# Kernel tuning notes

Hardware: AMD Instinct MI355X
Metric: run time of the kernel (lower is better)

Reference implementation:

```python
import jax, jax.numpy as jnp
import numpy as np

L, D, H, KS, VS, HID = 2048, 1024, 16, 1024, 1024, 4096
EPS = 1e-5


def _linear_params(key, din, dout):
    # torch nn.Linear default init: U(-1/sqrt(din), 1/sqrt(din))
    s = 1.0 / np.sqrt(din)
    kw, kb = jax.random.split(key)
    W = jax.random.uniform(kw, (dout, din), minval=-s, maxval=s, dtype=jnp.float32)
    b = jax.random.uniform(kb, (dout,), minval=-s, maxval=s, dtype=jnp.float32)
    return W, b


def setup_inputs() -> dict:
    key = jax.random.key(0)
    ks = jax.random.split(key, 12)
    x = jax.random.normal(ks[0], (L, D), dtype=jnp.float32)
    # inverse shortest-path lengths in [0, 1]
    shortest_path = jax.random.uniform(ks[1], (L, L), dtype=jnp.float32)
    Wq, bq = _linear_params(ks[2], D, KS)
    Wk, bk = _linear_params(ks[3], D, KS)
    Wv, bv = _linear_params(ks[4], D, VS)
    Wqp, bqp = _linear_params(ks[5], KS, KS)
    Wkp, bkp = _linear_params(ks[6], KS, KS)
    Wvp, bvp = _linear_params(ks[7], VS, VS)
    Wo, bo = _linear_params(ks[8], VS, D)
    W1, b1 = _linear_params(ks[9], D, HID)
    W2, b2 = _linear_params(ks[10], HID, D)
    g1 = jnp.ones((D,), jnp.float32); be1 = jnp.zeros((D,), jnp.float32)
    g2 = jnp.ones((D,), jnp.float32); be2 = jnp.zeros((D,), jnp.float32)
    return dict(x=x, shortest_path=shortest_path,
                Wq=Wq, bq=bq, Wk=Wk, bk=bk, Wv=Wv, bv=bv,
                Wqp=Wqp, bqp=bqp, Wkp=Wkp, bkp=bkp, Wvp=Wvp, bvp=bvp,
                Wo=Wo, bo=bo, W1=W1, b1=b1, W2=W2, b2=b2,
                g1=g1, be1=be1, g2=g2, be2=be2)


def _dense(h, W, b):
    return h @ W.T + b


def _layernorm(h, g, b):
    mu = jnp.mean(h, axis=-1, keepdims=True)
    var = jnp.mean(jnp.square(h - mu), axis=-1, keepdims=True)
    return (h - mu) * jax.lax.rsqrt(var + EPS) * g + b


def reference(x, shortest_path, Wq, bq, Wk, bk, Wv, bv, Wqp, bqp, Wkp, bkp,
              Wvp, bvp, Wo, bo, W1, b1, W2, b2, g1, be1, g2, be2):
    hd = KS // H
    vhd = VS // H
    q = _dense(_dense(x, Wq, bq), Wqp, bqp).reshape(L, H, hd).transpose(1, 0, 2)   # [H,L,hd]
    k = _dense(_dense(x, Wk, bk), Wkp, bkp).reshape(L, H, hd).transpose(1, 0, 2)   # [H,L,hd]
    v = _dense(_dense(x, Wv, bv), Wvp, bvp).reshape(L, H, vhd).transpose(1, 0, 2)  # [H,L,vhd]
    att = jnp.einsum('hld,hmd->hlm', q, k) / jnp.sqrt(jnp.float32(hd))             # [H,L,L]
    sp_bias = jax.nn.softmax(shortest_path, axis=-1) * 0.5                          # [L,L]
    att = jax.nn.softmax(att + sp_bias[None, :, :], axis=-1)
    o = jnp.einsum('hlm,hmd->hld', att, v).transpose(1, 0, 2).reshape(L, VS)        # [L,VS]
    o = _dense(o, Wo, bo)
    h = _layernorm(x + o, g1, be1)                # residual + LN1 (dropout=identity)
    f = jax.nn.relu(_dense(jax.nn.relu(_dense(h, W1, b1)), W2, b2))
    return _layernorm(h + f, g2, be2)             # residual + LN2
```

## Files before the change

### kernel.cpp

```cpp
#include <hip/hip_runtime.h>

typedef __attribute__((ext_vector_type(4))) float f32x4;
typedef __attribute__((ext_vector_type(8))) short s16x8;

static __device__ __forceinline__ ushort f2b(float f) {
  union { float f; unsigned u; } v; v.f = f;
  unsigned u = v.u;
  unsigned r = (u + 0x7fffu + ((u >> 16) & 1u)) >> 16;
  return (ushort)r;
}
static __device__ __forceinline__ float b2f(ushort h) {
  union { unsigned u; float f; } v; v.u = ((unsigned)h) << 16;
  return v.f;
}
static __device__ __forceinline__ unsigned cvtpk(float a, float b) {
  unsigned r;
  asm("v_cvt_pk_bf16_f32 %0, %1, %2" : "=v"(r) : "v"(a), "v"(b));
  return r;
}
static __device__ __forceinline__ float exp2i(float x) {
  float r;
  asm("v_exp_f32 %0, %1" : "=v"(r) : "v"(x));
  return r;
}

static __device__ __forceinline__ void gload_lds16(const ushort* g, ushort* l) {
  __builtin_amdgcn_global_load_lds(
      (const __attribute__((address_space(1))) void*)g,
      (__attribute__((address_space(3))) void*)l, 16, 0, 0);
}

#define LOG2E 1.44269504f

struct Cvt7 {
  const float* src[7];
  ushort* dst[7];
  int n[7];
};
__global__ __launch_bounds__(256) void cvt_multi_k(Cvt7 a) {
  int e = blockIdx.y;
  int i = (blockIdx.x * 256 + threadIdx.x) * 4;
  if (i >= a.n[e]) return;
  float4 v4 = *(const float4*)(a.src[e] + i);
  ushort4 o4; o4.x = f2b(v4.x); o4.y = f2b(v4.y); o4.z = f2b(v4.z); o4.w = f2b(v4.w);
  *(ushort4*)(a.dst[e] + i) = o4;
}

__global__ __launch_bounds__(256) void wtr_k(const float* __restrict__ Wq,
                                             const float* __restrict__ Wk,
                                             const float* __restrict__ Wv,
                                             ushort* __restrict__ dst) {
  __shared__ float t[64][65];
  int z = blockIdx.z;
  const float* src = z == 0 ? Wq : (z == 1 ? Wk : Wv);
  float scale = z == 0 ? 0.125f * LOG2E : 1.f;
  int r0 = blockIdx.x * 64, c0 = blockIdx.y * 64;
  int lr = threadIdx.x >> 2, lc4 = (threadIdx.x & 3) * 16;
#pragma unroll
  for (int j = 0; j < 4; ++j)
    *(float4*)&t[lr][lc4 + j * 4] = *(const float4*)(src + (size_t)(r0 + lr) * 1024 + c0 + lc4 + j * 4);
  __syncthreads();
  ushort tmp[16];
#pragma unroll
  for (int j = 0; j < 16; ++j) tmp[j] = f2b(t[lc4 + j][lr] * scale);
  ushort* d = dst + (size_t)z * 1048576 + (size_t)(c0 + lr) * 1024 + r0 + lc4;
  *(uint4*)d = *(uint4*)tmp;
  *(uint4*)(d + 8) = *(uint4*)(tmp + 8);
}

__global__ __launch_bounds__(256) void bvec_k(
    const float* __restrict__ Wqp, const float* __restrict__ Wkp, const float* __restrict__ Wvp,
    const float* __restrict__ bq, const float* __restrict__ bqp,
    const float* __restrict__ bk, const float* __restrict__ bkp,
    const float* __restrict__ bv, const float* __restrict__ bvp,
    float* __restrict__ outb) {
  int r = blockIdx.x * 4 + (threadIdx.x >> 6);
  int lane = threadIdx.x & 63;
  int z = r >> 10, rr = r & 1023;
  const float* Wp = z == 0 ? Wqp : (z == 1 ? Wkp : Wvp);
  const float* bi = z == 0 ? bq : (z == 1 ? bk : bv);
  const float* bp = z == 0 ? bqp : (z == 1 ? bkp : bvp);
  float s = 0.f;
#pragma unroll
  for (int t = 0; t < 4; ++t) {
    float4 w = *(const float4*)(Wp + (size_t)rr * 1024 + lane * 16 + t * 4);
    float4 b = *(const float4*)(bi + lane * 16 + t * 4);
    s += w.x * b.x + w.y * b.y + w.z * b.z + w.w * b.w;
  }
#pragma unroll
  for (int m = 1; m < 64; m <<= 1) s += __shfl_xor(s, m);
  if (lane == 0) outb[r] = (s + bp[rr]) * (z == 0 ? 0.125f * LOG2E : 1.f);
}

__global__ __launch_bounds__(256) void spsm_k(const float* __restrict__ sp,
                                              ushort* __restrict__ outP) {
  const int Lc = 2048;
  int row = blockIdx.x;
  int tid = threadIdx.x;
  const float* r = sp + (size_t)row * Lc;
  float v[8];
  float mx = -1e30f;
#pragma unroll
  for (int j = 0; j < 8; ++j) { v[j] = r[tid + j * 256]; mx = fmaxf(mx, v[j]); }
#pragma unroll
  for (int m = 1; m < 64; m <<= 1) mx = fmaxf(mx, __shfl_xor(mx, m));
  __shared__ float redm[4], reds[4];
  if ((tid & 63) == 0) redm[tid >> 6] = mx;
  __syncthreads();
  mx = fmaxf(fmaxf(redm[0], redm[1]), fmaxf(redm[2], redm[3]));
  float s = 0.f;
#pragma unroll
  for (int j = 0; j < 8; ++j) { v[j] = __expf(v[j] - mx); s += v[j]; }
#pragma unroll
  for (int m = 1; m < 64; m <<= 1) s += __shfl_xor(s, m);
  if ((tid & 63) == 0) reds[tid >> 6] = s;
  __syncthreads();
  s = reds[0] + reds[1] + reds[2] + reds[3];
  float inv = 0.5f * LOG2E / s;
  int mb = row >> 6, rr = row & 63;
  int wv = rr >> 4, rem = rr & 15, rg = rem >> 2, ii = rem & 3;
  size_t rbase = ((size_t)mb * 32) * 4096 + (size_t)wv * 1024 + (size_t)ii * 256 + (size_t)rg * 16;
#pragma unroll
  for (int j = 0; j < 8; ++j) {
    int col = tid + j * 256;
    int nb = col >> 6, cc = col & 63, nt = cc >> 4, cl = cc & 15;
    outP[rbase + (size_t)nb * 4096 + nt * 64 + cl] = f2b(v[j] * inv);
  }
}

__global__ __launch_bounds__(256) void vtr_k(const ushort* __restrict__ qkv,
                                             ushort* __restrict__ vT) {
  __shared__ ushort t[64][72];
  int tid = threadIdx.x;
  int r = tid >> 3, c8 = (tid & 7) * 8;
  int l0 = blockIdx.x * 64, h = blockIdx.y;
#pragma unroll
  for (int p = 0; p < 2; ++p)
    *(uint4*)&t[r + p * 32][c8] =
        *(const uint4*)(qkv + (size_t)(l0 + r + p * 32) * 3072 + 2048 + h * 64 + c8);
  __syncthreads();
#pragma unroll
  for (int p = 0; p < 2; ++p) {
    int d = r + p * 32;
    ushort tmp[8];
#pragma unroll
    for (int j = 0; j < 8; ++j) tmp[j] = t[c8 + j][d];
    *(uint4*)(vT + ((size_t)h * 64 + d) * 2048 + l0 + c8) = *(uint4*)tmp;
  }
}

template <int BM, int ZM>
__global__ __launch_bounds__(256, BM == 64 ? 3 : 2) void gemm_k(
    const ushort* __restrict__ A, const ushort* __restrict__ W,
    const float* __restrict__ bias, void* __restrict__ Cv,
    int M, int N, int K, int relu, float oscale) {
  constexpr int MT = BM / 32;
  __shared__ ushort As0[BM][64], Bs0[128][64];
  __shared__ ushort As1[BM][64], Bs1[128][64];
  const int z = (ZM != 0) ? blockIdx.z : 0;
  if (ZM == 1) { A += (size_t)z * M * K; W += (size_t)z * N * K; }
  int kb0 = 0, kb1 = K;
  if (ZM == 2) { int kh = K >> 1; kb0 = z * kh; kb1 = kb0 + kh; }
  const int tid = threadIdx.x;
  const int lane = tid & 63;
  const int wave = tid >> 6;
  const int wm = (wave >> 1) * (BM / 2);
  const int wn = (wave & 1) * 64;
  const int bm = blockIdx.x * BM;
  const int bn = blockIdx.y * 128;
  const int cl = lane & 15, rg = lane >> 4;
  const int lrow = lane >> 3, lcol = (lane & 7) * 8;

  f32x4 acc[MT][4];
#pragma unroll
  for (int i = 0; i < MT; ++i)
#pragma unroll
    for (int j = 0; j < 4; ++j) acc[i][j] = (f32x4){0.f, 0.f, 0.f, 0.f};

  const ushort* gA = A + (size_t)(bm + wave * 8 + lrow) * K + lcol;
  const ushort* gB = W + (size_t)(bn + wave * 8 + lrow) * K + lcol;

  auto stage = [&](ushort* lA, ushort* lB, int k0) {
#pragma unroll
    for (int c = 0; c < MT; ++c)
      gload_lds16(gA + (size_t)(c * 32) * K + k0, lA + wave * 512 + c * 2048);
#pragma unroll
    for (int c = 0; c < 4; ++c)
      gload_lds16(gB + (size_t)(c * 32) * K + k0, lB + wave * 512 + c * 2048);
  };
  auto compute = [&](const ushort* As, const ushort* Bs) {
    const int kbo = 8 * rg;
#pragma unroll
    for (int kk = 0; kk < 64; kk += 32) {
      s16x8 af[MT], bf[4];
#pragma unroll
      for (int mt = 0; mt < MT; ++mt)
        af[mt] = *(const s16x8*)(As + (wm + mt * 16 + cl) * 64 + kk + kbo);
#pragma unroll
      for (int nt = 0; nt < 4; ++nt)
        bf[nt] = *(const s16x8*)(Bs + (wn + nt * 16 + cl) * 64 + kk + kbo);
#pragma unroll
      for (int mt = 0; mt < MT; ++mt)
#pragma unroll
        for (int nt = 0; nt < 4; ++nt)
          acc[mt][nt] = __builtin_amdgcn_mfma_f32_16x16x32_bf16(af[mt], bf[nt], acc[mt][nt], 0, 0, 0);
    }
  };

  const int ktiles = (kb1 - kb0) >> 6;
  stage(&As0[0][0], &Bs0[0][0], kb0);
  __syncthreads();
  for (int tt = 0; tt < ktiles; tt += 2) {
    stage(&As1[0][0], &Bs1[0][0], kb0 + (tt + 1) * 64);
    compute(&As0[0][0], &Bs0[0][0]);
    __syncthreads();
    if (tt + 2 < ktiles) stage(&As0[0][0], &Bs0[0][0], kb0 + (tt + 2) * 64);
    compute(&As1[0][0], &Bs1[0][0]);
    __syncthreads();
  }

  if (ZM == 2) {
    float* Cf = (float*)Cv + (size_t)z * M * N;
#pragma unroll
    for (int nt = 0; nt < 4; ++nt) {
      int c = bn + wn + nt * 16 + cl;
#pragma unroll
      for (int mt = 0; mt < MT; ++mt)
#pragma unroll
        for (int i = 0; i < 4; ++i) {
          int r = bm + wm + mt * 16 + rg * 4 + i;
          Cf[(size_t)r * N + c] = acc[mt][nt][i];
        }
    }
  } else {
    ushort* Cu = (ushort*)Cv;
    if (ZM == 1) Cu += (size_t)z * M * N;
#pragma unroll
    for (int nt = 0; nt < 4; ++nt) {
      int c = bn + wn + nt * 16 + cl;
      float bv = bias ? bias[c] : 0.f;
#pragma unroll
      for (int mt = 0; mt < MT; ++mt) {
        float v0 = (acc[mt][nt][0] + bv) * oscale;
        float v1 = (acc[mt][nt][1] + bv) * oscale;
        float v2 = (acc[mt][nt][2] + bv) * oscale;
        float v3 = (acc[mt][nt][3] + bv) * oscale;
        if (relu) {
          v0 = fmaxf(v0, 0.f); v1 = fmaxf(v1, 0.f);
          v2 = fmaxf(v2, 0.f); v3 = fmaxf(v3, 0.f);
        }
        unsigned p01 = cvtpk(v0, v1), p23 = cvtpk(v2, v3);
        size_t b = (size_t)(bm + wm + mt * 16 + rg * 4) * N + c;
        Cu[b] = (ushort)p01;
        Cu[b + N] = (ushort)(p01 >> 16);
        Cu[b + 2 * N] = (ushort)p23;
        Cu[b + 3 * N] = (ushort)(p23 >> 16);
      }
    }
  }
}

__global__ __launch_bounds__(256, 4) void attn_k(
    const ushort* __restrict__ qkv, const ushort* __restrict__ vT,
    const ushort* __restrict__ biasP, ushort* __restrict__ opart,
    float* __restrict__ lbuf) {
  const int Lc = 2048;
  int h = blockIdx.x;
  int m0 = blockIdx.y * 128;
  int s = blockIdx.z;
  int nb = s * 512, ne = nb + 512;
  int tid = threadIdx.x, lane = tid & 63, wave = tid >> 6;

  __shared__ ushort Ks[64][72];
  __shared__ ushort Vs[64][72];
  __shared__ ushort Ps[4][2][16][72];

  const int rg = lane >> 4, cl = lane & 15;
  const int kb = 8 * rg;
  int srow = tid >> 3, scol = (tid & 7) * 8;

  s16x8 qfr[2][2];
#pragma unroll
  for (int mh = 0; mh < 2; ++mh) {
    const ushort* qp = qkv + (size_t)(m0 + mh * 64 + wave * 16 + cl) * 3072 + h * 64;
    qfr[mh][0] = *(const s16x8*)(qp + kb);
    qfr[mh][1] = *(const s16x8*)(qp + 32 + kb);
  }

  const ushort* bpB0 = biasP + ((size_t)(m0 >> 6) * 32) * 4096 + (size_t)wave * 1024 + lane;
  const ushort* bpB1 = bpB0 + (size_t)32 * 4096;

  f32x4 oacc[2][4];
#pragma unroll
  for (int mh = 0; mh < 2; ++mh)
#pragma unroll
    for (int i = 0; i < 4; ++i) oacc[mh][i] = (f32x4){0.f, 0.f, 0.f, 0.f};
  float lacc[2][4] = {{0.f, 0.f, 0.f, 0.f}, {0.f, 0.f, 0.f, 0.f}};

  for (int n0 = nb; n0 < ne; n0 += 64) {
    __syncthreads();
#pragma unroll
    for (int pp = 0; pp < 2; ++pp) {
      int r = srow + pp * 32;
      *(uint4*)&Ks[r][scol] = *(const uint4*)(qkv + (size_t)(n0 + r) * 3072 + 1024 + h * 64 + scol);
      *(uint4*)&Vs[r][scol] = *(const uint4*)(vT + ((size_t)h * 64 + r) * 2048 + n0 + scol);
    }
    __syncthreads();

#pragma unroll
    for (int mh = 0; mh < 2; ++mh) {
      const ushort* bp = (mh ? bpB1 : bpB0) + (size_t)(n0 >> 6) * 4096;
      f32x4 sacc[4];
#pragma unroll
      for (int i = 0; i < 4; ++i)
#pragma unroll
        for (int nt = 0; nt < 4; ++nt)
          sacc[nt][i] = b2f(bp[(i * 4 + nt) * 64]);

      __builtin_amdgcn_s_setprio(1);
#pragma unroll
      for (int kk2 = 0; kk2 < 2; ++kk2) {
#pragma unroll
        for (int nt = 0; nt < 4; ++nt) {
          s16x8 b = *(const s16x8*)&Ks[nt * 16 + cl][kk2 * 32 + kb];
          sacc[nt] = __builtin_amdgcn_mfma_f32_16x16x32_bf16(qfr[mh][kk2], b, sacc[nt], 0, 0, 0);
        }
      }
      __builtin_amdgcn_s_setprio(0);

#pragma unroll
      for (int i = 0; i < 4; ++i) {
#pragma unroll
        for (int nt = 0; nt < 4; ++nt) {
          float pv = exp2i(sacc[nt][i]);
          sacc[nt][i] = pv;
          lacc[mh][i] += pv;
        }
      }
#pragma unroll
      for (int nt = 0; nt < 4; ++nt) {
        unsigned p01 = cvtpk(sacc[nt][0], sacc[nt][1]);
        unsigned p23 = cvtpk(sacc[nt][2], sacc[nt][3]);
        Ps[wave][mh][rg * 4 + 0][nt * 16 + cl] = (ushort)p01;
        Ps[wave][mh][rg * 4 + 1][nt * 16 + cl] = (ushort)(p01 >> 16);
        Ps[wave][mh][rg * 4 + 2][nt * 16 + cl] = (ushort)p23;
        Ps[wave][mh][rg * 4 + 3][nt * 16 + cl] = (ushort)(p23 >> 16);
      }
    }

    __builtin_amdgcn_s_setprio(1);
#pragma unroll
    for (int mh = 0; mh < 2; ++mh) {
#pragma unroll
      for (int kk = 0; kk < 64; kk += 32) {
        s16x8 a = *(const s16x8*)&Ps[wave][mh][cl][kk + kb];
#pragma unroll
        for (int nt = 0; nt < 4; ++nt) {
          s16x8 b = *(const s16x8*)&Vs[nt * 16 + cl][kk + kb];
          oacc[mh][nt] = __builtin_amdgcn_mfma_f32_16x16x32_bf16(a, b, oacc[mh][nt], 0, 0, 0);
        }
      }
    }
    __builtin_amdgcn_s_setprio(0);
  }

#pragma unroll
  for (int mh = 0; mh < 2; ++mh) {
#pragma unroll
    for (int nt = 0; nt < 4; ++nt) {
      unsigned p01 = cvtpk(oacc[mh][nt][0], oacc[mh][nt][1]);
      unsigned p23 = cvtpk(oacc[mh][nt][2], oacc[mh][nt][3]);
      size_t b = ((size_t)s * Lc + (m0 + mh * 64 + wave * 16 + rg * 4)) * 1024 + h * 64 + nt * 16 + cl;
      opart[b] = (ushort)p01;
      opart[b + 1024] = (ushort)(p01 >> 16);
      opart[b + 2048] = (ushort)p23;
      opart[b + 3072] = (ushort)(p23 >> 16);
    }
#pragma unroll
    for (int i = 0; i < 4; ++i) {
      float l = lacc[mh][i];
#pragma unroll
      for (int m = 1; m < 16; m <<= 1) l += __shfl_xor(l, m);
      if (cl == 0) {
        int r = m0 + mh * 64 + wave * 16 + rg * 4 + i;
        lbuf[(size_t)(s * 16 + h) * Lc + r] = l;
      }
    }
  }
}

__global__ __launch_bounds__(256) void acomb_k(const ushort* __restrict__ op,
                                               const float* __restrict__ lbuf,
                                               ushort* __restrict__ ob) {
  const int Lc = 2048;
  int qrow = blockIdx.x;
  int tid = threadIdx.x;
  int c = tid * 4;
  int h = c >> 6;
  float lsum = 0.f;
#pragma unroll
  for (int s = 0; s < 4; ++s) lsum += lbuf[(size_t)(s * 16 + h) * Lc + qrow];
  float inv = 1.f / lsum;
  float acc0 = 0.f, acc1 = 0.f, acc2 = 0.f, acc3 = 0.f;
#pragma unroll
  for (int s = 0; s < 4; ++s) {
    ushort4 a = *(const ushort4*)(op + ((size_t)s * Lc + qrow) * 1024 + c);
    acc0 += b2f(a.x); acc1 += b2f(a.y); acc2 += b2f(a.z); acc3 += b2f(a.w);
  }
  ushort4 o;
  o.x = f2b(acc0 * inv); o.y = f2b(acc1 * inv);
  o.z = f2b(acc2 * inv); o.w = f2b(acc3 * inv);
  *(ushort4*)(ob + (size_t)qrow * 1024 + c) = o;
}

__global__ __launch_bounds__(256) void lnf_k(const float* __restrict__ basef,
                                             const float* __restrict__ p,
                                             const float* __restrict__ bvec,
                                             const float* __restrict__ g,
                                             const float* __restrict__ be,
                                             int relu,
                                             ushort* __restrict__ outb,
                                             float* __restrict__ outf) {
  const int Dc = 1024;
  const size_t MN = (size_t)2048 * 1024;
  int row = blockIdx.x;
  int tid = threadIdx.x;
  int c = tid * 4;
  float4 bx = *(const float4*)(basef + (size_t)row * Dc + c);
  float4 a0 = *(const float4*)(p + (size_t)row * Dc + c);
  float4 a1 = *(const float4*)(p + MN + (size_t)row * Dc + c);
  float4 bb = *(const float4*)(bvec + c);
  float v0 = a0.x + a1.x + bb.x, v1 = a0.y + a1.y + bb.y;
  float v2 = a0.z + a1.z + bb.z, v3 = a0.w + a1.w + bb.w;
  if (relu) {
    v0 = fmaxf(v0, 0.f); v1 = fmaxf(v1, 0.f);
    v2 = fmaxf(v2, 0.f); v3 = fmaxf(v3, 0.f);
  }
  v0 += bx.x; v1 += bx.y; v2 += bx.z; v3 += bx.w;
  float s = v0 + v1 + v2 + v3;
  __shared__ float red[4];
#pragma unroll
  for (int m = 1; m < 64; m <<= 1) s += __shfl_xor(s, m);
  if ((tid & 63) == 0) red[tid >> 6] = s;
  __syncthreads();
  s = red[0] + red[1] + red[2] + red[3];
  float mu = s * (1.f / Dc);
  float d0 = v0 - mu, d1 = v1 - mu, d2 = v2 - mu, d3 = v3 - mu;
  float ss = d0 * d0 + d1 * d1 + d2 * d2 + d3 * d3;
  __syncthreads();
#pragma unroll
  for (int m = 1; m < 64; m <<= 1) ss += __shfl_xor(ss, m);
  if ((tid & 63) == 0) red[tid >> 6] = ss;
  __syncthreads();
  ss = red[0] + red[1] + red[2] + red[3];
  float rs = rsqrtf(ss * (1.f / Dc) + 1e-5f);
  float4 gv = *(const float4*)(g + c);
  float4 bev = *(const float4*)(be + c);
  float y0 = d0 * rs * gv.x + bev.x;
  float y1 = d1 * rs * gv.y + bev.y;
  float y2 = d2 * rs * gv.z + bev.z;
  float y3 = d3 * rs * gv.w + bev.w;
  size_t o = (size_t)row * Dc + c;
  if (outb) {
    ushort4 ob4; ob4.x = f2b(y0); ob4.y = f2b(y1); ob4.z = f2b(y2); ob4.w = f2b(y3);
    *(ushort4*)(outb + o) = ob4;
  }
  if (outf) {
    float4 of4; of4.x = y0; of4.y = y1; of4.z = y2; of4.w = y3;
    *(float4*)(outf + o) = of4;
  }
}

extern "C" void kernel_launch(void* const* d_in, const int* in_sizes, int n_in,
                              void* d_out, int out_size, void* d_ws, size_t ws_size,
                              hipStream_t stream) {
  const int L = 2048, D = 1024, H = 16, HID = 4096;
  const float* x   = (const float*)d_in[0];
  const float* sp  = (const float*)d_in[1];
  const float* Wq  = (const float*)d_in[2];  const float* bq  = (const float*)d_in[3];
  const float* Wk  = (const float*)d_in[4];  const float* bk  = (const float*)d_in[5];
  const float* Wv  = (const float*)d_in[6];  const float* bv  = (const float*)d_in[7];
  const float* Wqp = (const float*)d_in[8];  const float* bqp = (const float*)d_in[9];
  const float* Wkp = (const float*)d_in[10]; const float* bkp = (const float*)d_in[11];
  const float* Wvp = (const float*)d_in[12]; const float* bvp = (const float*)d_in[13];
  const float* Wo  = (const float*)d_in[14]; const float* bo  = (const float*)d_in[15];
  const float* W1  = (const float*)d_in[16]; const float* b1  = (const float*)d_in[17];
  const float* W2  = (const float*)d_in[18]; const float* b2  = (const float*)d_in[19];
  const float* g1  = (const float*)d_in[20]; const float* be1 = (const float*)d_in[21];
  const float* g2  = (const float*)d_in[22]; const float* be2 = (const float*)d_in[23];
  float* out = (float*)d_out;

  size_t off = 0;
  char* base = (char*)d_ws;
  auto alloc = [&](size_t b) {
    char* p = base + off;
    off += (b + 255) & ~(size_t)255;
    return p;
  };
  ushort* xb    = (ushort*)alloc((size_t)L * D * 2);
  ushort* wqpb  = (ushort*)alloc((size_t)D * D * 2);
  ushort* wkpb  = (ushort*)alloc((size_t)D * D * 2);
  ushort* wvpb  = (ushort*)alloc((size_t)D * D * 2);
  ushort* wqTb  = (ushort*)alloc((size_t)3 * D * D * 2);
  ushort* wfused= (ushort*)alloc((size_t)3 * D * D * 2);
  ushort* qkv   = (ushort*)alloc((size_t)L * 3072 * 2);
  float*  bfused= (float*)alloc((size_t)3072 * 4);
  ushort* wob   = (ushort*)alloc((size_t)D * D * 2);
  ushort* w1b   = (ushort*)alloc((size_t)HID * D * 2);
  ushort* w2b   = (ushort*)alloc((size_t)D * HID * 2);
  ushort* spsb  = (ushort*)alloc((size_t)L * L * 2);
  ushort* opart = (ushort*)alloc((size_t)4 * L * 1024 * 2);
  ushort* vT    = (ushort*)alloc((size_t)H * 64 * L * 2);
  float*  lbuf  = (float*)alloc((size_t)4 * H * L * 4);
  ushort* ob    = (ushort*)alloc((size_t)L * 1024 * 2);
  ushort* hb    = (ushort*)alloc((size_t)L * D * 2);
  float*  hf    = (float*)alloc((size_t)L * D * 4);

  ushort* ffn1  = wqTb;
  float*  parts = (float*)spsb;

  Cvt7 ca;
  ca.src[0] = x;   ca.dst[0] = xb;   ca.n[0] = L * D;
  ca.src[1] = Wqp; ca.dst[1] = wqpb; ca.n[1] = D * D;
  ca.src[2] = Wkp; ca.dst[2] = wkpb; ca.n[2] = D * D;
  ca.src[3] = Wvp; ca.dst[3] = wvpb; ca.n[3] = D * D;
  ca.src[4] = Wo;  ca.dst[4] = wob;  ca.n[4] = D * D;
  ca.src[5] = W1;  ca.dst[5] = w1b;  ca.n[5] = HID * D;
  ca.src[6] = W2;  ca.dst[6] = w2b;  ca.n[6] = D * HID;
  cvt_multi_k<<<dim3(4096, 7), dim3(256), 0, stream>>>(ca);

  wtr_k<<<dim3(16, 16, 3), dim3(256), 0, stream>>>(Wq, Wk, Wv, wqTb);
  bvec_k<<<dim3(768), dim3(256), 0, stream>>>(Wqp, Wkp, Wvp, bq, bqp, bk, bkp, bv, bvp, bfused);
  spsm_k<<<dim3(L), dim3(256), 0, stream>>>(sp, spsb);

  gemm_k<64, 1><<<dim3(16, 8, 3), dim3(256), 0, stream>>>(
      wqpb, wqTb, (const float*)nullptr, wfused, D, D, D, 0, 1.f);
  gemm_k<64, 0><<<dim3(32, 24), dim3(256), 0, stream>>>(
      xb, wfused, bfused, qkv, L, 3072, D, 0, 1.f);

  vtr_k<<<dim3(L / 64, H), dim3(256), 0, stream>>>(qkv, vT);
  attn_k<<<dim3(H, L / 128, 4), dim3(256), 0, stream>>>(qkv, vT, spsb, opart, lbuf);
  acomb_k<<<dim3(L), dim3(256), 0, stream>>>(opart, lbuf, ob);

  gemm_k<64, 2><<<dim3(32, 8, 2), dim3(256), 0, stream>>>(
      ob, wob, (const float*)nullptr, parts, L, D, D, 0, 1.f);
  lnf_k<<<dim3(L), dim3(256), 0, stream>>>(x, parts, bo, g1, be1, 0, hb, hf);
  gemm_k<128, 0><<<dim3(16, 32), dim3(256), 0, stream>>>(
      hb, w1b, b1, ffn1, L, HID, D, 1, 1.f);
  gemm_k<64, 2><<<dim3(32, 8, 2), dim3(256), 0, stream>>>(
      ffn1, w2b, (const float*)nullptr, parts, L, D, HID, 0, 1.f);
  lnf_k<<<dim3(L), dim3(256), 0, stream>>>(hf, parts, b2, g2, be2, 1, (ushort*)nullptr, out);
}
```

Measured before the change: 212.6 us.

## Use 4-way split-K with bf16 partials and smaller FFN1 tiles

After: 215.3 us. No clear change (+1.3%).

```diff
diff --git a/kernel.cpp b/kernel.cpp
--- a/kernel.cpp
+++ b/kernel.cpp
@@ -160,7 +160,7 @@
   const int z = (ZM != 0) ? blockIdx.z : 0;
   if (ZM == 1) { A += (size_t)z * M * K; W += (size_t)z * N * K; }
   int kb0 = 0, kb1 = K;
-  if (ZM == 2) { int kh = K >> 1; kb0 = z * kh; kb1 = kb0 + kh; }
+  if (ZM == 2) { int kh = K >> 2; kb0 = z * kh; kb1 = kb0 + kh; }
   const int tid = threadIdx.x;
   const int lane = tid & 63;
   const int wave = tid >> 6;
@@ -219,43 +219,30 @@
     __syncthreads();
   }
 
-  if (ZM == 2) {
-    float* Cf = (float*)Cv + (size_t)z * M * N;
-#pragma unroll
-    for (int nt = 0; nt < 4; ++nt) {
-      int c = bn + wn + nt * 16 + cl;
-#pragma unroll
-      for (int mt = 0; mt < MT; ++mt)
-#pragma unroll
-        for (int i = 0; i < 4; ++i) {
-          int r = bm + wm + mt * 16 + rg * 4 + i;
-          Cf[(size_t)r * N + c] = acc[mt][nt][i];
-        }
-    }
-  } else {
-    ushort* Cu = (ushort*)Cv;
-    if (ZM == 1) Cu += (size_t)z * M * N;
-#pragma unroll
-    for (int nt = 0; nt < 4; ++nt) {
-      int c = bn + wn + nt * 16 + cl;
-      float bv = bias ? bias[c] : 0.f;
-#pragma unroll
-      for (int mt = 0; mt < MT; ++mt) {
-        float v0 = (acc[mt][nt][0] + bv) * oscale;
-        float v1 = (acc[mt][nt][1] + bv) * oscale;
-        float v2 = (acc[mt][nt][2] + bv) * oscale;
-        float v3 = (acc[mt][nt][3] + bv) * oscale;
-        if (relu) {
-          v0 = fmaxf(v0, 0.f); v1 = fmaxf(v1, 0.f);
-          v2 = fmaxf(v2, 0.f); v3 = fmaxf(v3, 0.f);
-        }
-        unsigned p01 = cvtpk(v0, v1), p23 = cvtpk(v2, v3);
-        size_t b = (size_t)(bm + wm + mt * 16 + rg * 4) * N + c;
-        Cu[b] = (ushort)p01;
-        Cu[b + N] = (ushort)(p01 >> 16);
-        Cu[b + 2 * N] = (ushort)p23;
-        Cu[b + 3 * N] = (ushort)(p23 >> 16);
+  ushort* Cu = (ushort*)Cv;
+  if (ZM != 0) Cu += (size_t)z * M * N;
+  float bscale = (ZM == 2) ? 0.f : 1.f;
+#pragma unroll
+  for (int nt = 0; nt < 4; ++nt) {
+    int c = bn + wn + nt * 16 + cl;
+    float bv = (bias && ZM != 2) ? bias[c] : 0.f;
+    (void)bscale;
+#pragma unroll
+    for (int mt = 0; mt < MT; ++mt) {
+      float v0 = (acc[mt][nt][0] + bv) * oscale;
+      float v1 = (acc[mt][nt][1] + bv) * oscale;
+      float v2 = (acc[mt][nt][2] + bv) * oscale;
+      float v3 = (acc[mt][nt][3] + bv) * oscale;
+      if (relu) {
+        v0 = fmaxf(v0, 0.f); v1 = fmaxf(v1, 0.f);
+        v2 = fmaxf(v2, 0.f); v3 = fmaxf(v3, 0.f);
       }
+      unsigned p01 = cvtpk(v0, v1), p23 = cvtpk(v2, v3);
+      size_t b = (size_t)(bm + wm + mt * 16 + rg * 4) * N + c;
+      Cu[b] = (ushort)p01;
+      Cu[b + N] = (ushort)(p01 >> 16);
+      Cu[b + 2 * N] = (ushort)p23;
+      Cu[b + 3 * N] = (ushort)(p23 >> 16);
     }
   }
 }
@@ -414,7 +401,7 @@
 }
 
 __global__ __launch_bounds__(256) void lnf_k(const float* __restrict__ basef,
-                                             const float* __restrict__ p,
+                                             const ushort* __restrict__ p,
                                              const float* __restrict__ bvec,
                                              const float* __restrict__ g,
                                              const float* __restrict__ be,
@@ -427,11 +414,13 @@
   int tid = threadIdx.x;
   int c = tid * 4;
   float4 bx = *(const float4*)(basef + (size_t)row * Dc + c);
-  float4 a0 = *(const float4*)(p + (size_t)row * Dc + c);
-  float4 a1 = *(const float4*)(p + MN + (size_t)row * Dc + c);
   float4 bb = *(const float4*)(bvec + c);
-  float v0 = a0.x + a1.x + bb.x, v1 = a0.y + a1.y + bb.y;
-  float v2 = a0.z + a1.z + bb.z, v3 = a0.w + a1.w + bb.w;
+  float v0 = bb.x, v1 = bb.y, v2 = bb.z, v3 = bb.w;
+#pragma unroll
+  for (int s = 0; s < 4; ++s) {
+    ushort4 a = *(const ushort4*)(p + s * MN + (size_t)row * Dc + c);
+    v0 += b2f(a.x); v1 += b2f(a.y); v2 += b2f(a.z); v3 += b2f(a.w);
+  }
   if (relu) {
     v0 = fmaxf(v0, 0.f); v1 = fmaxf(v1, 0.f);
     v2 = fmaxf(v2, 0.f); v3 = fmaxf(v3, 0.f);
@@ -517,7 +506,7 @@
   float*  hf    = (float*)alloc((size_t)L * D * 4);
 
   ushort* ffn1  = wqTb;
-  float*  parts = (float*)spsb;
+  ushort* parts = opart;
 
   Cvt7 ca;
   ca.src[0] = x;   ca.dst[0] = xb;   ca.n[0] = L * D;
@@ -542,12 +531,12 @@
   attn_k<<<dim3(H, L / 128, 4), dim3(256), 0, stream>>>(qkv, vT, spsb, opart, lbuf);
   acomb_k<<<dim3(L), dim3(256), 0, stream>>>(opart, lbuf, ob);
 
-  gemm_k<64, 2><<<dim3(32, 8, 2), dim3(256), 0, stream>>>(
+  gemm_k<64, 2><<<dim3(32, 8, 4), dim3(256), 0, stream>>>(
       ob, wob, (const float*)nullptr, parts, L, D, D, 0, 1.f);
   lnf_k<<<dim3(L), dim3(256), 0, stream>>>(x, parts, bo, g1, be1, 0, hb, hf);
-  gemm_k<128, 0><<<dim3(16, 32), dim3(256), 0, stream>>>(
+  gemm_k<64, 0><<<dim3(32, 32), dim3(256), 0, stream>>>(
       hb, w1b, b1, ffn1, L, HID, D, 1, 1.f);
-  gemm_k<64, 2><<<dim3(32, 8, 2), dim3(256), 0, stream>>>(
+  gemm_k<64, 2><<<dim3(32, 8, 4), dim3(256), 0, stream>>>(
       ffn1, w2b, (const float*)nullptr, parts, L, D, HID, 0, 1.f);
   lnf_k<<<dim3(L), dim3(256), 0, stream>>>(hf, parts, b2, g2, be2, 1, (ushort*)nullptr, out);
 }
```
